# Kernel optimization log

Measured on AMD Instinct MI355X. Metric: run time of the kernel, lower is better.

## Reference

```python
import jax, jax.numpy as jnp
import numpy as np

C = 256
H = W = 80
PATCH = 3  # patchsize, stride 1 -> npatches = (H-2)*(W-2) = 6084


def setup_inputs() -> dict:
    key = jax.random.key(0)
    k_style, k_x = jax.random.split(key)
    style = jax.random.normal(k_style, (1, C, H, W), jnp.float32)
    # torch: activation.unfold(2,3,1).unfold(3,3,1).squeeze() -> (C, nH, nW, 3, 3)
    #        .permute(1,2,0,3,4).view(nH*nW, C, 3, 3)
    s = np.asarray(style)
    win = np.lib.stride_tricks.sliding_window_view(s, (PATCH, PATCH), axis=(2, 3))  # (1,C,78,78,3,3)
    patches = np.ascontiguousarray(win[0].transpose(1, 2, 0, 3, 4).reshape(-1, C, PATCH, PATCH))
    x = jax.random.normal(k_x, (1, C, H, W), jnp.float32)
    return {"x": x, "patches": jnp.asarray(patches)}


def reference(x, patches):
    # NOTE: the original's per-patch normalization uses .mul (not .mul_), a no-op,
    # so conv_enc weight == raw patches, same as conv_dec. Replicated here.
    npatches = patches.shape[0]
    dn = ("NCHW", "OIHW", "NCHW")
    # conv_enc: valid 3x3 conv, patches as filters -> (1, npatches, 78, 78)
    sim = jax.lax.conv_general_dilated(x, patches, (1, 1), "VALID", dimension_numbers=dn)
    # per-pixel argmax over patch channel + one-hot (replaces the python double loop)
    idx = jnp.argmax(sim, axis=1)  # (1, 78, 78)
    onehot = jax.nn.one_hot(idx, npatches, axis=1, dtype=x.dtype)  # (1, npatches, 78, 78)
    # conv_dec / aux: ConvTranspose2d == adjoint of the valid conv (transpose_kernel=True)
    swap = jax.lax.conv_transpose(onehot, patches, (1, 1), "VALID", dimension_numbers=dn, transpose_kernel=True)
    swap_wei = jax.lax.conv_transpose(onehot, jnp.ones_like(patches), (1, 1), "VALID", dimension_numbers=dn, transpose_kernel=True)
    return swap / swap_wei  # (1, C, 80, 80)
```

## Files before the change

### kernel.cpp

```cpp
#include <hip/hip_runtime.h>
#include <stdint.h>

#define NPIX 6084
#define NPAD 6144
#define KDIM 2304
#define KB   (KDIM*2)
#define NT   36

typedef __attribute__((ext_vector_type(8))) short s16x8;
typedef __attribute__((ext_vector_type(4))) float f32x4;

__device__ __forceinline__ short f2bf(float f) {
  unsigned u = __builtin_bit_cast(unsigned, f);
  u += 0x7FFFu + ((u >> 16) & 1u);
  return (short)(u >> 16);
}
__device__ __forceinline__ float bf2f(short s) {
  unsigned u = ((unsigned)(unsigned short)s) << 16;
  return __builtin_bit_cast(float, u);
}

#define GL16(g, l)                                                            \
  __builtin_amdgcn_global_load_lds(                                           \
      (__attribute__((address_space(1))) unsigned int*)(g),                   \
      (__attribute__((address_space(3))) unsigned int*)(l), 16, 0, 0)

__global__ __launch_bounds__(256) void k_prep_pat(const float* __restrict__ pat,
                                                  short* __restrict__ out) {
  int i = blockIdx.x * 256 + threadIdx.x;
  int e0 = i * 8;
  int row = e0 / KDIM;
  s16x8 v;
  if (row < NPIX) {
    const float* s = pat + e0;
#pragma unroll
    for (int j = 0; j < 8; ++j) v[j] = f2bf(s[j]);
  } else {
#pragma unroll
    for (int j = 0; j < 8; ++j) v[j] = 0;
  }
  *(s16x8*)(out + e0) = v;
}

__global__ __launch_bounds__(256) void k_prep_xcol(const float* __restrict__ x,
                                                   short* __restrict__ out) {
  int i = blockIdx.x * 256 + threadIdx.x;
  int e0 = i * 8;
  int m = e0 / KDIM;
  int k0 = e0 - m * KDIM;
  s16x8 v;
  if (m < NPIX) {
    int p = m / 78, q = m - p * 78;
#pragma unroll
    for (int j = 0; j < 8; ++j) {
      int k = k0 + j;
      int c = k / 9;
      int r = k - c * 9;
      int dy = r / 3, dx = r - dy * 3;
      v[j] = f2bf(x[c * 6400 + (p + dy) * 80 + (q + dx)]);
    }
  } else {
#pragma unroll
    for (int j = 0; j < 8; ++j) v[j] = 0;
  }
  *(s16x8*)(out + e0) = v;
}

__global__ __launch_bounds__(512, 2) void k_gemm(const short* __restrict__ A,
                                                 const short* __restrict__ B,
                                                 short* __restrict__ C) {
  __shared__ __align__(1024) char smem[131072];
  const int tid = threadIdx.x;
  const int w = tid >> 6, lane = tid & 63;
  const int wr = w >> 2, wc = w & 3;
  const int tm = blockIdx.y, tn = blockIdx.x;
  const char* Ab = (const char*)A + (size_t)tm * 256 * KB;
  const char* Bb = (const char*)B + (size_t)tn * 256 * KB;

  const int srccol = ((lane & 7) * 16) ^ ((lane >> 3) << 4);
  const int lrow = lane >> 3;
  const int fragRow = lane & 15;
  const int swz = (lane & 7) << 4;
  const int colb0 = (lane >> 4) * 16;
  const int aOff = (wr * 128 + fragRow) * 128;
  const int bOff = 32768 + (wc * 64 + fragRow) * 128;

  f32x4 acc[8][4] = {};
  s16x8 a[4][2];
  s16x8 b[2][2][2];

#define STAGE_A(par, hs, kt)                                                  \
  _Pragma("unroll") for (int j = 0; j < 2; ++j) {                             \
    int c = w * 2 + j;                                                        \
    int rb = (c < 8) ? (hs)*64 + c * 8 : 128 + (hs)*64 + (c - 8) * 8;         \
    GL16(Ab + (size_t)(rb + lrow) * KB + (kt)*128 + srccol,                   \
         smem + (par)*65536 + rb * 128);                                      \
  }
#define STAGE_B(par, hs, kt)                                                  \
  _Pragma("unroll") for (int j = 0; j < 2; ++j) {                             \
    int c = w * 2 + j;                                                        \
    int rb = (c >> 2) * 64 + (hs)*32 + (c & 3) * 8;                           \
    GL16(Bb + (size_t)(rb + lrow) * KB + (kt)*128 + srccol,                   \
         smem + (par)*65536 + 32768 + rb * 128);                              \
  }
#define LDA(par, mh)                                                          \
  _Pragma("unroll") for (int mi2 = 0; mi2 < 4; ++mi2)                         \
  _Pragma("unroll") for (int ks = 0; ks < 2; ++ks)                            \
    a[mi2][ks] = *(const s16x8*)(smem + (par)*65536 + aOff + (mh)*8192 +      \
                                 mi2 * 2048 + ((colb0 + ks * 64) ^ swz));
#define LDB(par, nh)                                                          \
  _Pragma("unroll") for (int ni2 = 0; ni2 < 2; ++ni2)                         \
  _Pragma("unroll") for (int ks = 0; ks < 2; ++ks)                            \
    b[nh][ni2][ks] = *(const s16x8*)(smem + (par)*65536 + bOff + (nh)*4096 +  \
                                     ni2 * 2048 + ((colb0 + ks * 64) ^ swz));
#define VM6() asm volatile("s_waitcnt vmcnt(6)" ::: "memory")
#define BAR() asm volatile("s_barrier" ::: "memory")
#define BARL() asm volatile("s_barrier\n\ts_waitcnt lgkmcnt(0)" ::: "memory")
#define QM(mh, nh)                                                            \
  do {                                                                        \
    __builtin_amdgcn_s_setprio(1);                                            \
    _Pragma("unroll") for (int mi2 = 0; mi2 < 4; ++mi2)                       \
    _Pragma("unroll") for (int ni2 = 0; ni2 < 2; ++ni2)                       \
    _Pragma("unroll") for (int ks = 0; ks < 2; ++ks)                          \
      acc[(mh)*4 + mi2][(nh)*2 + ni2] =                                       \
          __builtin_amdgcn_mfma_f32_16x16x32_bf16(                            \
              a[mi2][ks], b[nh][ni2][ks], acc[(mh)*4 + mi2][(nh)*2 + ni2],    \
              0, 0, 0);                                                       \
    __builtin_amdgcn_s_setprio(0);                                            \
    BAR();                                                                    \
  } while (0)

  STAGE_A(0, 0, 0); STAGE_B(0, 0, 0); STAGE_B(0, 1, 0); STAGE_A(0, 1, 0);
  STAGE_A(1, 0, 1); STAGE_B(1, 0, 1); STAGE_B(1, 1, 1);
  VM6();
  BAR();

#pragma unroll 1
  for (int i = 0; i < NT / 2; ++i) {
    const int t2 = (2 * i + 2 < NT) ? 2 * i + 2 : NT - 1;
    const int t3 = (2 * i + 3 < NT) ? 2 * i + 3 : NT - 1;
    LDA(0, 0); LDB(0, 0);
    STAGE_A(1, 1, 2 * i + 1);
    BARL(); QM(0, 0);
    LDB(0, 1);
    STAGE_A(0, 0, t2);
    BARL(); QM(0, 1);
    LDA(0, 1);
    STAGE_B(0, 0, t2);
    BARL(); QM(1, 1);
    STAGE_B(0, 1, t2);
    VM6();
    BARL(); QM(1, 0);
    LDA(1, 0); LDB(1, 0);
    STAGE_A(0, 1, t2);
    BARL(); QM(0, 0);
    LDB(1, 1);
    STAGE_A(1, 0, t3);
    BARL(); QM(0, 1);
    LDA(1, 1);
    STAGE_B(1, 0, t3);
    BARL(); QM(1, 1);
    STAGE_B(1, 1, t3);
    VM6();
    BARL(); QM(1, 0);
  }

  const int rowb = tm * 256 + wr * 128 + (lane >> 4) * 4;
  const int colb = tn * 256 + wc * 64 + (lane & 15);
#pragma unroll
  for (int mi = 0; mi < 8; ++mi)
#pragma unroll
    for (int ni = 0; ni < 4; ++ni)
#pragma unroll
      for (int j = 0; j < 4; ++j)
        C[(size_t)(rowb + mi * 16 + j) * NPAD + colb + ni * 16] =
            f2bf(acc[mi][ni][j]);
}

__global__ __launch_bounds__(256) void k_argmax(const short* __restrict__ sim,
                                                const float* __restrict__ x,
                                                const float* __restrict__ pat,
                                                int* __restrict__ amax) {
  __shared__ int cand[4][32];
  __shared__ int ccnt[4];
  const int tid = threadIdx.x, w = tid >> 6, lane = tid & 63;
  const int pix = blockIdx.x * 4 + w;
  const short* row = sim + (size_t)pix * NPAD;

  float best = -1e30f;
  int bidx = 0;
  for (int it = 0; it < 12; ++it) {
    int k0 = (it * 64 + lane) * 8;
    if (k0 < NPIX) {
      s16x8 v = *(const s16x8*)(row + k0);
#pragma unroll
      for (int j = 0; j < 8; ++j) {
        int k = k0 + j;
        float f = bf2f(v[j]);
        if (k < NPIX && (f > best || (f == best && k < bidx))) {
          best = f; bidx = k;
        }
      }
    }
  }
  for (int off = 32; off; off >>= 1) {
    float ov = __shfl_down(best, off);
    int oi = __shfl_down(bidx, off);
    if (ov > best || (ov == best && oi < bidx)) { best = ov; bidx = oi; }
  }
  float maxv = __shfl(best, 0);

  if (lane == 0) ccnt[w] = 0;
  __syncthreads();

  const float thr = maxv - 4.0f;
  for (int it = 0; it < 12; ++it) {
    int k0 = (it * 64 + lane) * 8;
    if (k0 < NPIX) {
      s16x8 v = *(const s16x8*)(row + k0);
#pragma unroll
      for (int j = 0; j < 8; ++j) {
        int k = k0 + j;
        float f = bf2f(v[j]);
        if (k < NPIX && f >= thr) {
          int pos = atomicAdd(&ccnt[w], 1);
          if (pos < 32) cand[w][pos] = k;
        }
      }
    }
  }
  __syncthreads();

  int n = ccnt[w] < 32 ? ccnt[w] : 32;
  const int p = pix / 78, q = pix - (pix / 78) * 78;
  double bests = -1e300;
  int bestk = 0;
  for (int ci = 0; ci < n; ++ci) {
    int k = cand[w][ci];
    double s = 0.0;
    for (int cc = lane; cc < 256; cc += 64) {
      const float* xb = x + cc * 6400 + p * 80 + q;
      const float* pb = pat + (size_t)k * KDIM + cc * 9;
#pragma unroll
      for (int dy = 0; dy < 3; ++dy)
#pragma unroll
        for (int dx = 0; dx < 3; ++dx)
          s += (double)xb[dy * 80 + dx] * (double)pb[dy * 3 + dx];
    }
    for (int off = 32; off; off >>= 1) s += __shfl_down(s, off);
    if (lane == 0 && (s > bests || (s == bests && k < bestk))) {
      bests = s; bestk = k;
    }
  }
  if (lane == 0) amax[pix] = bestk;
}

__global__ __launch_bounds__(256) void k_scat9(const float* __restrict__ pat,
                                               const int* __restrict__ amax,
                                               float* __restrict__ plane) {
  __shared__ float lp[KDIM];
  const int b = blockIdx.x;
  const int k = amax[b];
  const int p = b / 78, q = b - (b / 78) * 78;
  const float* src = pat + (size_t)k * KDIM;
#pragma unroll
  for (int j = 0; j < 9; ++j) lp[j * 256 + threadIdx.x] = src[j * 256 + threadIdx.x];
  __syncthreads();
  const int c = threadIdx.x;
#pragma unroll
  for (int r = 0; r < 9; ++r) {
    int dy = r / 3, dx = r - dy * 3;
    int pos = (p + dy) * 80 + (q + dx);
    plane[(size_t)r * 1638400 + pos * 256 + c] = lp[c * 9 + r];
  }
}

__global__ __launch_bounds__(256) void k_reduce(const float* __restrict__ plane,
                                                float* __restrict__ out) {
  const int c = threadIdx.x;
  const int pix0 = blockIdx.x * 16;
  for (int i = 0; i < 16; ++i) {
    int pix = pix0 + i;
    int yy = pix / 80, xx = pix - (pix / 80) * 80;
    float s = 0.f;
    int cnt = 0;
#pragma unroll
    for (int r = 0; r < 9; ++r) {
      int dy = r / 3, dx = r - dy * 3;
      int p = yy - dy, q = xx - dx;
      if (p >= 0 && p < 78 && q >= 0 && q < 78) {
        s += plane[(size_t)r * 1638400 + pix * 256 + c];
        ++cnt;
      }
    }
    out[c * 6400 + pix] = s / (float)cnt;
  }
}

extern "C" void kernel_launch(void* const* d_in, const int* in_sizes, int n_in,
                              void* d_out, int out_size, void* d_ws,
                              size_t ws_size, hipStream_t stream) {
  const float* x = (const float*)d_in[0];
  const float* pat = (const float*)d_in[1];
  float* out = (float*)d_out;
  char* ws = (char*)d_ws;

  short* patB = (short*)ws;
  short* xcol = (short*)(ws + 28311552);
  short* sim  = (short*)(ws + 2 * 28311552);
  float* plane = (float*)sim;
  int*   amax = (int*)(ws + 2 * 28311552 + 75497472);

  k_prep_pat<<<6912, 256, 0, stream>>>(pat, patB);
  k_prep_xcol<<<6912, 256, 0, stream>>>(x, xcol);
  k_gemm<<<dim3(24, 24), 512, 0, stream>>>(xcol, patB, sim);
  k_argmax<<<1521, 256, 0, stream>>>(sim, x, pat, amax);
  k_scat9<<<6084, 256, 0, stream>>>(pat, amax, plane);
  k_reduce<<<400, 256, 0, stream>>>(plane, out);
}
```

Baseline: 437.3 us.

## Fuse per-tile argmax into GEMM epilogue and rewrite im2col with LDS staging

The GEMM epilogue now computes a per-row argmax within each 256-column tile and writes it to small gval/gidx arrays. The argmax kernel merges those 24 tile maxima and rescans only the sim tiles whose max is within the threshold, instead of reading full 6144-wide rows twice. It also skips the fp64 refinement when there is at most one candidate. The im2col kernel stages input rows in shared memory so global reads are coalesced, at the cost of a barrier and extra epilogue work in the GEMM.

```diff
diff --git a/kernel.cpp b/kernel.cpp
--- a/kernel.cpp
+++ b/kernel.cpp
@@ -42,33 +42,40 @@
   *(s16x8*)(out + e0) = v;
 }
 
-__global__ __launch_bounds__(256) void k_prep_xcol(const float* __restrict__ x,
-                                                   short* __restrict__ out) {
-  int i = blockIdx.x * 256 + threadIdx.x;
-  int e0 = i * 8;
-  int m = e0 / KDIM;
-  int k0 = e0 - m * KDIM;
-  s16x8 v;
-  if (m < NPIX) {
-    int p = m / 78, q = m - p * 78;
-#pragma unroll
-    for (int j = 0; j < 8; ++j) {
-      int k = k0 + j;
-      int c = k / 9;
-      int r = k - c * 9;
-      int dy = r / 3, dx = r - dy * 3;
-      v[j] = f2bf(x[c * 6400 + (p + dy) * 80 + (q + dx)]);
-    }
-  } else {
-#pragma unroll
-    for (int j = 0; j < 8; ++j) v[j] = 0;
-  }
-  *(s16x8*)(out + e0) = v;
+__global__ __launch_bounds__(256) void k_xcol2(const float* __restrict__ x,
+                                               short* __restrict__ out) {
+  __shared__ float lx[7680];
+  const int b = blockIdx.x, tid = threadIdx.x;
+  if (b >= 624) {
+    int i = b - 624;
+    s16x8 z = {};
+#pragma unroll
+    for (int it = 0; it < 9; ++it) {
+      int t = i * 2160 + it * 256 + tid;
+      if (t < 17280) ((s16x8*)out)[(size_t)NPIX * KDIM / 8 + t] = z;
+    }
+    return;
+  }
+  const int p = b >> 3, cc = b & 7;
+  for (int t = tid; t < 7680; t += 256) {
+    int ci = t / 240, rr = t - ci * 240;
+    lx[t] = x[(cc * 32 + ci) * 6400 + p * 80 + rr];
+  }
+  __syncthreads();
+  for (int t = tid; t < 22464; t += 256) {
+    int q = t / 288, e = t - q * 288;
+    int ci = e / 9, r = e - ci * 9;
+    int dy = r / 3, dx = r - dy * 3;
+    out[(size_t)(p * 78 + q) * KDIM + cc * 288 + e] =
+        f2bf(lx[ci * 240 + dy * 80 + q + dx]);
+  }
 }
 
 __global__ __launch_bounds__(512, 2) void k_gemm(const short* __restrict__ A,
                                                  const short* __restrict__ B,
-                                                 short* __restrict__ C) {
+                                                 short* __restrict__ C,
+                                                 float* __restrict__ gval,
+                                                 int* __restrict__ gidx) {
   __shared__ __align__(1024) char smem[131072];
   const int tid = threadIdx.x;
   const int w = tid >> 6, lane = tid & 63;
@@ -175,54 +182,84 @@
       for (int j = 0; j < 4; ++j)
         C[(size_t)(rowb + mi * 16 + j) * NPAD + colb + ni * 16] =
             f2bf(acc[mi][ni][j]);
-}
-
-__global__ __launch_bounds__(256) void k_argmax(const short* __restrict__ sim,
-                                                const float* __restrict__ x,
-                                                const float* __restrict__ pat,
-                                                int* __restrict__ amax) {
+
+  float* tval = (float*)smem;
+  int* tcol = (int*)(smem + 4096);
+#pragma unroll
+  for (int mi = 0; mi < 8; ++mi)
+#pragma unroll
+    for (int j = 0; j < 4; ++j) {
+      float bv = -1e30f;
+      int bc = 0x7FFFFFFF;
+#pragma unroll
+      for (int ni = 0; ni < 4; ++ni) {
+        int cg = colb + ni * 16;
+        float v = (cg < NPIX) ? acc[mi][ni][j] : -1e30f;
+        if (v > bv || (v == bv && cg < bc)) { bv = v; bc = cg; }
+      }
+#pragma unroll
+      for (int off = 1; off < 16; off <<= 1) {
+        float ov = __shfl_xor(bv, off);
+        int oc = __shfl_xor(bc, off);
+        if (ov > bv || (ov == bv && oc < bc)) { bv = ov; bc = oc; }
+      }
+      if ((lane & 15) == 0) {
+        int rloc = wr * 128 + mi * 16 + (lane >> 4) * 4 + j;
+        tval[rloc * 4 + wc] = bv;
+        tcol[rloc * 4 + wc] = bc;
+      }
+    }
+  __syncthreads();
+  if (tid < 256) {
+    float bv = tval[tid * 4];
+    int bc = tcol[tid * 4];
+#pragma unroll
+    for (int t = 1; t < 4; ++t) {
+      float v = tval[tid * 4 + t];
+      int c2 = tcol[tid * 4 + t];
+      if (v > bv || (v == bv && c2 < bc)) { bv = v; bc = c2; }
+    }
+    gval[tn * NPAD + tm * 256 + tid] = bv;
+    gidx[tn * NPAD + tm * 256 + tid] = bc;
+  }
+}
+
+__global__ __launch_bounds__(256) void k_argmax2(const short* __restrict__ sim,
+                                                 const float* __restrict__ gval,
+                                                 const int* __restrict__ gidx,
+                                                 const float* __restrict__ x,
+                                                 const float* __restrict__ pat,
+                                                 int* __restrict__ amax) {
   __shared__ int cand[4][32];
   __shared__ int ccnt[4];
   const int tid = threadIdx.x, w = tid >> 6, lane = tid & 63;
   const int pix = blockIdx.x * 4 + w;
-  const short* row = sim + (size_t)pix * NPAD;
-
-  float best = -1e30f;
-  int bidx = 0;
-  for (int it = 0; it < 12; ++it) {
-    int k0 = (it * 64 + lane) * 8;
-    if (k0 < NPIX) {
-      s16x8 v = *(const s16x8*)(row + k0);
-#pragma unroll
-      for (int j = 0; j < 8; ++j) {
-        int k = k0 + j;
-        float f = bf2f(v[j]);
-        if (k < NPIX && (f > best || (f == best && k < bidx))) {
-          best = f; bidx = k;
-        }
-      }
-    }
-  }
+
+  float v0 = (lane < 24) ? gval[lane * NPAD + pix] : -1e30f;
+  int c0 = (lane < 24) ? gidx[lane * NPAD + pix] : 0x7FFFFFFF;
+  float v = v0;
+  int c = c0;
   for (int off = 32; off; off >>= 1) {
-    float ov = __shfl_down(best, off);
-    int oi = __shfl_down(bidx, off);
-    if (ov > best || (ov == best && oi < bidx)) { best = ov; bidx = oi; }
-  }
-  float maxv = __shfl(best, 0);
+    float ov = __shfl_down(v, off);
+    int oc = __shfl_down(c, off);
+    if (ov > v || (ov == v && oc < c)) { v = ov; c = oc; }
+  }
+  const float maxv = __shfl(v, 0);
+  const int bestc = __shfl(c, 0);
 
   if (lane == 0) ccnt[w] = 0;
   __syncthreads();
 
-  const float thr = maxv - 4.0f;
-  for (int it = 0; it < 12; ++it) {
-    int k0 = (it * 64 + lane) * 8;
-    if (k0 < NPIX) {
-      s16x8 v = *(const s16x8*)(row + k0);
-#pragma unroll
-      for (int j = 0; j < 8; ++j) {
-        int k = k0 + j;
-        float f = bf2f(v[j]);
-        if (k < NPIX && f >= thr) {
+  const float thrb = maxv - 4.0f;
+  for (int t = 0; t < 24; ++t) {
+    float bm = __shfl(v0, t);
+    if (bm >= thrb) {
+      short4 s4 = *(const short4*)(sim + (size_t)pix * NPAD + t * 256 + lane * 4);
+#pragma unroll
+      for (int j = 0; j < 4; ++j) {
+        int k = t * 256 + lane * 4 + j;
+        float f = bf2f(((const short*)&s4)[j]);
+        if (f >= thrb - 0.6f && k < NPIX) {
           int pos = atomicAdd(&ccnt[w], 1);
           if (pos < 32) cand[w][pos] = k;
         }
@@ -232,6 +269,10 @@
   __syncthreads();
 
   int n = ccnt[w] < 32 ? ccnt[w] : 32;
+  if (n <= 1) {
+    if (lane == 0) amax[pix] = bestc;
+    return;
+  }
   const int p = pix / 78, q = pix - (pix / 78) * 78;
   double bests = -1e300;
   int bestk = 0;
@@ -309,12 +350,14 @@
   short* xcol = (short*)(ws + 28311552);
   short* sim  = (short*)(ws + 2 * 28311552);
   float* plane = (float*)sim;
-  int*   amax = (int*)(ws + 2 * 28311552 + 75497472);
+  int*   amax = (int*)(ws + 132120576);
+  float* gval = (float*)(ws + 132144912);
+  int*   gidx = (int*)(ws + 132734736);
 
   k_prep_pat<<<6912, 256, 0, stream>>>(pat, patB);
-  k_prep_xcol<<<6912, 256, 0, stream>>>(x, xcol);
-  k_gemm<<<dim3(24, 24), 512, 0, stream>>>(xcol, patB, sim);
-  k_argmax<<<1521, 256, 0, stream>>>(sim, x, pat, amax);
+  k_xcol2<<<632, 256, 0, stream>>>(x, xcol);
+  k_gemm<<<dim3(24, 24), 512, 0, stream>>>(xcol, patB, sim, gval, gidx);
+  k_argmax2<<<1521, 256, 0, stream>>>(sim, gval, gidx, x, pat, amax);
   k_scat9<<<6084, 256, 0, stream>>>(pat, amax, plane);
   k_reduce<<<400, 256, 0, stream>>>(plane, out);
 }
```

New measurement: 442.1 us. No clear change (+1.1%).
